# Kernel tuning notes

Measured on AMD Instinct MI355X. Metric: run time of the kernel, lower is better.

## Reference

```python
import jax, jax.numpy as jnp
import numpy as np

B, IN_DIM, OUT_DIM = 4096, 4096, 4096

def setup_inputs() -> dict:
    key = jax.random.key(0)
    kx, kw, kb = jax.random.split(key, 3)
    x = jax.random.normal(kx, (B, IN_DIM), dtype=jnp.float32)
    W = jax.random.normal(kw, (OUT_DIM, IN_DIM), dtype=jnp.float32) * (1.0 / np.sqrt(IN_DIM))
    b = jax.random.normal(kb, (OUT_DIM,), dtype=jnp.float32) * (1.0 / np.sqrt(IN_DIM))
    return {"x": x, "W": W, "b": b}

def reference(x, W, b):
    # Original computes sum over in_dim of x[:, :, None] * W.T[None, :, :],
    # which is exactly x @ W.T. NOTE: bias is added TWICE in the source
    # (duplicated `out += self.b`), so the faithful output is x @ W.T + 2*b.
    out = jnp.einsum('bi,oi->bo', x, W)  # [B, out_dim]
    out = out + 2.0 * b
    return out
```

## Files before the change

### kernel.cpp

```cpp
#include <hip/hip_runtime.h>
#include <hip/hip_bf16.h>


typedef short bf16x8 __attribute__((ext_vector_type(8)));
typedef short s16x4  __attribute__((ext_vector_type(4)));
typedef short s16x8  __attribute__((ext_vector_type(8)));
typedef float f32x4  __attribute__((ext_vector_type(4)));

constexpr int MDIM = 4096, NDIM = 4096, KDIM = 4096;

typedef const __attribute__((address_space(1))) void* gas_t;
typedef __attribute__((address_space(3))) void*       las_t;

__device__ __forceinline__ short f2bf(float f) {
    __hip_bfloat16 h = __float2bfloat16(f);
    short s; __builtin_memcpy(&s, &h, 2); return s;
}

__global__ __launch_bounds__(256)
void cvt_f32_bf16(const float* __restrict__ in, short* __restrict__ out, int n8) {
    int idx    = blockIdx.x * blockDim.x + threadIdx.x;
    int stride = gridDim.x * blockDim.x;
    const f32x4* in4 = (const f32x4*)in;
    s16x8* out8 = (s16x8*)out;
    for (int i = idx; i < n8; i += stride) {
        f32x4 a = in4[2 * i];
        f32x4 b = in4[2 * i + 1];
        s16x8 o = { f2bf(a[0]), f2bf(a[1]), f2bf(a[2]), f2bf(a[3]),
                    f2bf(b[0]), f2bf(b[1]), f2bf(b[2]), f2bf(b[3]) };
        out8[i] = o;
    }
}

constexpr int BM = 256, BN = 256, BK = 64;
constexpr int NT  = KDIM / BK;
constexpr int ASZ = BM * BK;
constexpr int BSZ = BN * BK;

template <int Q, class StageFn>
__device__ __forceinline__ void phase(const short* Ab, int rA, int c0, int c1,
                                      bf16x8 (&bf)[4][2], f32x4 (&acc)[8][4],
                                      StageFn&& stage) {
    bf16x8 af[2][2];
    #pragma unroll
    for (int m = 0; m < 2; ++m) {
        const short* p = &Ab[(rA + Q * 32 + m * 16) * BK];
        af[m][0] = *(const bf16x8*)(p + c0);
        af[m][1] = *(const bf16x8*)(p + c1);
    }
    stage();
    __builtin_amdgcn_s_barrier();
    __builtin_amdgcn_s_setprio(1);
    #pragma unroll
    for (int m = 0; m < 2; ++m)
        #pragma unroll
        for (int ni = 0; ni < 4; ++ni)
            #pragma unroll
            for (int kk = 0; kk < 2; ++kk)
                acc[Q * 2 + m][ni] = __builtin_amdgcn_mfma_f32_16x16x32_bf16(
                    af[m][kk], bf[ni][kk], acc[Q * 2 + m][ni], 0, 0, 0);
    __builtin_amdgcn_s_setprio(0);
}

__global__ __launch_bounds__(512, 2)
void gemm_bf16_256(const short* __restrict__ Xb, const short* __restrict__ Wb,
                   const float* __restrict__ Bv, float* __restrict__ Out)
{
    __shared__ short lds[2 * ASZ + 2 * BSZ];

    const int tid  = threadIdx.x;
    const int lane = tid & 63;
    const int wid  = tid >> 6;
    const int wr   = wid >> 2;
    const int wc   = wid & 3;

    const int bid = blockIdx.x;
    const int lin = (bid & 7) * 32 + (bid >> 3);
    const int tm0 = (lin >> 4) * BM;
    const int tn0 = (lin & 15) * BN;

    const int srow = lane >> 3;
    const int sgrn = (lane & 7) ^ srow;
    const short* aSrc[2][2];
    const short* bSrc[2][2];
    int dOff[2][2];
    #pragma unroll
    for (int h = 0; h < 2; ++h) {
        #pragma unroll
        for (int j = 0; j < 2; ++j) {
            const int r = h * 128 + (2 * wid + j) * 8;
            aSrc[h][j] = Xb + (size_t)(tm0 + r + srow) * KDIM + sgrn * 8;
            bSrc[h][j] = Wb + (size_t)(tn0 + r + srow) * KDIM + sgrn * 8;
            dOff[h][j] = r * BK;
        }
    }
    auto stageA = [&](int kt, int h) {
        short* dst = (short*)&lds[(kt & 1) * ASZ];
        __builtin_amdgcn_global_load_lds((gas_t)(aSrc[h][0] + (size_t)kt * BK),
                                         (las_t)(dst + dOff[h][0]), 16, 0, 0);
        __builtin_amdgcn_global_load_lds((gas_t)(aSrc[h][1] + (size_t)kt * BK),
                                         (las_t)(dst + dOff[h][1]), 16, 0, 0);
    };
    auto stageB = [&](int kt, int h) {
        short* dst = (short*)&lds[2 * ASZ + (kt & 1) * BSZ];
        __builtin_amdgcn_global_load_lds((gas_t)(bSrc[h][0] + (size_t)kt * BK),
                                         (las_t)(dst + dOff[h][0]), 16, 0, 0);
        __builtin_amdgcn_global_load_lds((gas_t)(bSrc[h][1] + (size_t)kt * BK),
                                         (las_t)(dst + dOff[h][1]), 16, 0, 0);
    };

    const int g   = lane >> 4;
    const int r16 = lane & 15;
    const int c0  = ((0 + g) ^ (r16 & 7)) * 8;
    const int c1  = ((4 + g) ^ (r16 & 7)) * 8;
    const int rA  = wr * 128 + r16;
    const int rB  = wc * 64  + r16;

    f32x4 acc[8][4] = {};

    stageB(0, 0); stageB(0, 1); stageA(0, 0); stageA(0, 1); stageB(1, 0); stageB(1, 1);
    asm volatile("s_waitcnt vmcnt(4)" ::: "memory");
    __builtin_amdgcn_s_barrier();
    __builtin_amdgcn_sched_barrier(0);

    for (int t = 0; t < NT; ++t) {
        const short* Ab = (const short*)&lds[(t & 1) * ASZ];
        const short* Bb = (const short*)&lds[2 * ASZ + (t & 1) * BSZ];

        bf16x8 bf[4][2];
        #pragma unroll
        for (int ni = 0; ni < 4; ++ni) {
            const short* p = &Bb[(rB + ni * 16) * BK];
            bf[ni][0] = *(const bf16x8*)(p + c0);
            bf[ni][1] = *(const bf16x8*)(p + c1);
        }
        phase<0>(Ab, rA, c0, c1, bf, acc, [&] { if (t + 1 < NT) stageA(t + 1, 0); });
        __builtin_amdgcn_s_barrier();
        phase<1>(Ab, rA, c0, c1, bf, acc, [&] { if (t + 1 < NT) stageA(t + 1, 1); });
        __builtin_amdgcn_s_barrier();
        phase<2>(Ab, rA, c0, c1, bf, acc, [&] { if (t + 2 < NT) stageB(t + 2, 0); });
        __builtin_amdgcn_s_barrier();
        phase<3>(Ab, rA, c0, c1, bf, acc, [&] { if (t + 2 < NT) stageB(t + 2, 1); });
        if (t < NT - 2)       { asm volatile("s_waitcnt vmcnt(4)" ::: "memory"); }
        else if (t == NT - 2) { asm volatile("s_waitcnt vmcnt(0)" ::: "memory"); }
        __builtin_amdgcn_s_barrier();
        __builtin_amdgcn_sched_barrier(0);
    }

    float bb[4];
    #pragma unroll
    for (int ni = 0; ni < 4; ++ni)
        bb[ni] = 2.0f * Bv[tn0 + wc * 64 + ni * 16 + r16];

    #pragma unroll
    for (int mi = 0; mi < 8; ++mi) {
        #pragma unroll
        for (int r = 0; r < 4; ++r) {
            const int row = tm0 + wr * 128 + mi * 16 + g * 4 + r;
            float* orow = Out + (size_t)row * NDIM + tn0 + wc * 64 + r16;
            #pragma unroll
            for (int ni = 0; ni < 4; ++ni)
                orow[ni * 16] = acc[mi][ni][r] + bb[ni];
        }
    }
}

constexpr int FBM = 128, FBN = 128, FBK = 32, LDT = FBK + 8;
__global__ __launch_bounds__(256)
void gemm_xwt_bias2(const float* __restrict__ X, const float* __restrict__ W,
                    const float* __restrict__ Bv, float* __restrict__ Out)
{
    __shared__ short As[FBM * LDT];
    __shared__ short Bs[FBN * LDT];
    const int tid  = threadIdx.x;
    const int lane = tid & 63;
    const int wid  = tid >> 6;
    const int wr   = wid >> 1;
    const int wc   = wid & 1;
    const int tm0  = blockIdx.y * FBM;
    const int tn0  = blockIdx.x * FBN;
    const int srow = tid >> 3;
    const int scol = (tid & 7) * 4;
    const int g    = lane >> 4;
    const int r16  = lane & 15;
    f32x4 acc[4][4] = {};
    const float* xg = X + (size_t)(tm0 + srow) * KDIM + scol;
    const float* wg = W + (size_t)(tn0 + srow) * KDIM + scol;
    for (int k0 = 0; k0 < KDIM; k0 += FBK) {
        #pragma unroll
        for (int i = 0; i < 4; ++i) {
            const int row = srow + 32 * i;
            f32x4 av = *(const f32x4*)(xg + (size_t)(32 * i) * KDIM + k0);
            f32x4 bv = *(const f32x4*)(wg + (size_t)(32 * i) * KDIM + k0);
            s16x4 pa = { f2bf(av[0]), f2bf(av[1]), f2bf(av[2]), f2bf(av[3]) };
            s16x4 pb = { f2bf(bv[0]), f2bf(bv[1]), f2bf(bv[2]), f2bf(bv[3]) };
            *(s16x4*)&As[row * LDT + scol] = pa;
            *(s16x4*)&Bs[row * LDT + scol] = pb;
        }
        __syncthreads();
        bf16x8 af[4], bfr[4];
        #pragma unroll
        for (int mi = 0; mi < 4; ++mi)
            af[mi] = *(const bf16x8*)&As[(wr * 64 + mi * 16 + r16) * LDT + g * 8];
        #pragma unroll
        for (int ni = 0; ni < 4; ++ni)
            bfr[ni] = *(const bf16x8*)&Bs[(wc * 64 + ni * 16 + r16) * LDT + g * 8];
        #pragma unroll
        for (int mi = 0; mi < 4; ++mi)
            #pragma unroll
            for (int ni = 0; ni < 4; ++ni)
                acc[mi][ni] = __builtin_amdgcn_mfma_f32_16x16x32_bf16(
                                  af[mi], bfr[ni], acc[mi][ni], 0, 0, 0);
        __syncthreads();
    }
    float bb[4];
    #pragma unroll
    for (int ni = 0; ni < 4; ++ni)
        bb[ni] = 2.0f * Bv[tn0 + wc * 64 + ni * 16 + r16];
    #pragma unroll
    for (int mi = 0; mi < 4; ++mi)
        #pragma unroll
        for (int r = 0; r < 4; ++r) {
            const int row = tm0 + wr * 64 + mi * 16 + g * 4 + r;
            float* orow = Out + (size_t)row * NDIM + tn0 + wc * 64 + r16;
            #pragma unroll
            for (int ni = 0; ni < 4; ++ni)
                orow[ni * 16] = acc[mi][ni][r] + bb[ni];
        }
}

extern "C" void kernel_launch(void* const* d_in, const int* in_sizes, int n_in,
                              void* d_out, int out_size, void* d_ws, size_t ws_size,
                              hipStream_t stream) {
    const float* X  = (const float*)d_in[0];
    const float* W  = (const float*)d_in[1];
    const float* Bv = (const float*)d_in[2];
    float* Out = (float*)d_out;

    const size_t nElem = (size_t)MDIM * KDIM;
    const size_t need  = 2 * nElem * sizeof(short);

    if (ws_size >= need) {
        short* Xb = (short*)d_ws;
        short* Wb = Xb + nElem;
        const int n8 = (int)(nElem / 8);
        cvt_f32_bf16<<<2048, 256, 0, stream>>>(X, Xb, n8);
        cvt_f32_bf16<<<2048, 256, 0, stream>>>(W, Wb, n8);
        gemm_bf16_256<<<dim3(256), 512, 0, stream>>>(Xb, Wb, Bv, Out);
    } else {
        dim3 grid(NDIM / FBN, MDIM / FBM);
        gemm_xwt_bias2<<<grid, 256, 0, stream>>>(X, W, Bv, Out);
    }
}
```

Before: 141.8 us.

## Switch GEMM to 32x32x16 MFMA tiles and fuse the two bf16 conversion kernels

The main GEMM now uses 32x32x16 bf16 MFMA instructions with 16-wide accumulators instead of 16x16x32, which cuts the number of LDS fragment reads per FLOP and the number of MFMA issues. The epilogue is rewritten for the 32x32 output layout. The two f32-to-bf16 conversion launches are merged into one kernel with a larger grid, saving one launch. The sched_barrier hints are dropped, which may change how the compiler interleaves LDS reads and MFMAs.

```diff
diff --git a/kernel.cpp b/kernel.cpp
--- a/kernel.cpp
+++ b/kernel.cpp
@@ -6,6 +6,7 @@
 typedef short s16x4  __attribute__((ext_vector_type(4)));
 typedef short s16x8  __attribute__((ext_vector_type(8)));
 typedef float f32x4  __attribute__((ext_vector_type(4)));
+typedef float f32x16 __attribute__((ext_vector_type(16)));
 
 constexpr int MDIM = 4096, NDIM = 4096, KDIM = 4096;
 
@@ -18,17 +19,19 @@
 }
 
 __global__ __launch_bounds__(256)
-void cvt_f32_bf16(const float* __restrict__ in, short* __restrict__ out, int n8) {
+void cvt2_f32_bf16(const float* __restrict__ inA, const float* __restrict__ inB,
+                   short* __restrict__ outA, short* __restrict__ outB, int n8each) {
     int idx    = blockIdx.x * blockDim.x + threadIdx.x;
     int stride = gridDim.x * blockDim.x;
-    const f32x4* in4 = (const f32x4*)in;
-    s16x8* out8 = (s16x8*)out;
-    for (int i = idx; i < n8; i += stride) {
-        f32x4 a = in4[2 * i];
-        f32x4 b = in4[2 * i + 1];
+    for (int i = idx; i < 2 * n8each; i += stride) {
+        const f32x4* in4 = (i < n8each) ? (const f32x4*)inA : (const f32x4*)inB;
+        s16x8*      out8 = (i < n8each) ? (s16x8*)outA      : (s16x8*)outB;
+        int j = (i < n8each) ? i : i - n8each;
+        f32x4 a = in4[2 * j];
+        f32x4 b = in4[2 * j + 1];
         s16x8 o = { f2bf(a[0]), f2bf(a[1]), f2bf(a[2]), f2bf(a[3]),
                     f2bf(b[0]), f2bf(b[1]), f2bf(b[2]), f2bf(b[3]) };
-        out8[i] = o;
+        out8[j] = o;
     }
 }
 
@@ -37,28 +40,24 @@
 constexpr int ASZ = BM * BK;
 constexpr int BSZ = BN * BK;
 
-template <int Q, class StageFn>
-__device__ __forceinline__ void phase(const short* Ab, int rA, int c0, int c1,
-                                      bf16x8 (&bf)[4][2], f32x4 (&acc)[8][4],
-                                      StageFn&& stage) {
-    bf16x8 af[2][2];
-    #pragma unroll
-    for (int m = 0; m < 2; ++m) {
-        const short* p = &Ab[(rA + Q * 32 + m * 16) * BK];
-        af[m][0] = *(const bf16x8*)(p + c0);
-        af[m][1] = *(const bf16x8*)(p + c1);
-    }
+template <int MF, class StageFn>
+__device__ __forceinline__ void phase32(const short* Ab, int rA, const int (&ck)[4],
+                                        bf16x8 (&bf)[2][4], f32x16 (&acc)[4][2],
+                                        StageFn&& stage) {
+    bf16x8 af[4];
+    const short* p = &Ab[(rA + MF * 32) * BK];
+    #pragma unroll
+    for (int s = 0; s < 4; ++s)
+        af[s] = *(const bf16x8*)(p + ck[s]);
     stage();
     __builtin_amdgcn_s_barrier();
     __builtin_amdgcn_s_setprio(1);
     #pragma unroll
-    for (int m = 0; m < 2; ++m)
-        #pragma unroll
-        for (int ni = 0; ni < 4; ++ni)
-            #pragma unroll
-            for (int kk = 0; kk < 2; ++kk)
-                acc[Q * 2 + m][ni] = __builtin_amdgcn_mfma_f32_16x16x32_bf16(
-                    af[m][kk], bf[ni][kk], acc[Q * 2 + m][ni], 0, 0, 0);
+    for (int nf = 0; nf < 2; ++nf)
+        #pragma unroll
+        for (int s = 0; s < 4; ++s)
+            acc[MF][nf] = __builtin_amdgcn_mfma_f32_32x32x16_bf16(
+                              af[s], bf[nf][s], acc[MF][nf], 0, 0, 0);
     __builtin_amdgcn_s_setprio(0);
 }
 
@@ -109,58 +108,60 @@
                                          (las_t)(dst + dOff[h][1]), 16, 0, 0);
     };
 
-    const int g   = lane >> 4;
-    const int r16 = lane & 15;
-    const int c0  = ((0 + g) ^ (r16 & 7)) * 8;
-    const int c1  = ((4 + g) ^ (r16 & 7)) * 8;
-    const int rA  = wr * 128 + r16;
-    const int rB  = wc * 64  + r16;
-
-    f32x4 acc[8][4] = {};
+    const int l31 = lane & 31;
+    const int g2  = lane >> 5;
+    int ck[4];
+    #pragma unroll
+    for (int s = 0; s < 4; ++s)
+        ck[s] = ((2 * s + g2) ^ (lane & 7)) * 8;
+    const int rA = wr * 128 + l31;
+    const int rB = wc * 64  + l31;
+
+    f32x16 acc[4][2] = {};
 
     stageB(0, 0); stageB(0, 1); stageA(0, 0); stageA(0, 1); stageB(1, 0); stageB(1, 1);
     asm volatile("s_waitcnt vmcnt(4)" ::: "memory");
     __builtin_amdgcn_s_barrier();
-    __builtin_amdgcn_sched_barrier(0);
 
     for (int t = 0; t < NT; ++t) {
         const short* Ab = (const short*)&lds[(t & 1) * ASZ];
         const short* Bb = (const short*)&lds[2 * ASZ + (t & 1) * BSZ];
 
-        bf16x8 bf[4][2];
-        #pragma unroll
-        for (int ni = 0; ni < 4; ++ni) {
-            const short* p = &Bb[(rB + ni * 16) * BK];
-            bf[ni][0] = *(const bf16x8*)(p + c0);
-            bf[ni][1] = *(const bf16x8*)(p + c1);
-        }
-        phase<0>(Ab, rA, c0, c1, bf, acc, [&] { if (t + 1 < NT) stageA(t + 1, 0); });
-        __builtin_amdgcn_s_barrier();
-        phase<1>(Ab, rA, c0, c1, bf, acc, [&] { if (t + 1 < NT) stageA(t + 1, 1); });
-        __builtin_amdgcn_s_barrier();
-        phase<2>(Ab, rA, c0, c1, bf, acc, [&] { if (t + 2 < NT) stageB(t + 2, 0); });
-        __builtin_amdgcn_s_barrier();
-        phase<3>(Ab, rA, c0, c1, bf, acc, [&] { if (t + 2 < NT) stageB(t + 2, 1); });
+        bf16x8 bf[2][4];
+        #pragma unroll
+        for (int nf = 0; nf < 2; ++nf) {
+            const short* p = &Bb[(rB + nf * 32) * BK];
+            #pragma unroll
+            for (int s = 0; s < 4; ++s)
+                bf[nf][s] = *(const bf16x8*)(p + ck[s]);
+        }
+        phase32<0>(Ab, rA, ck, bf, acc, [&] { if (t + 1 < NT) stageA(t + 1, 0); });
+        __builtin_amdgcn_s_barrier();
+        phase32<1>(Ab, rA, ck, bf, acc, [&] { if (t + 1 < NT) stageA(t + 1, 1); });
+        __builtin_amdgcn_s_barrier();
+        phase32<2>(Ab, rA, ck, bf, acc, [&] { if (t + 2 < NT) stageB(t + 2, 0); });
+        __builtin_amdgcn_s_barrier();
+        phase32<3>(Ab, rA, ck, bf, acc, [&] { if (t + 2 < NT) stageB(t + 2, 1); });
         if (t < NT - 2)       { asm volatile("s_waitcnt vmcnt(4)" ::: "memory"); }
         else if (t == NT - 2) { asm volatile("s_waitcnt vmcnt(0)" ::: "memory"); }
         __builtin_amdgcn_s_barrier();
-        __builtin_amdgcn_sched_barrier(0);
-    }
-
-    float bb[4];
-    #pragma unroll
-    for (int ni = 0; ni < 4; ++ni)
-        bb[ni] = 2.0f * Bv[tn0 + wc * 64 + ni * 16 + r16];
-
-    #pragma unroll
-    for (int mi = 0; mi < 8; ++mi) {
-        #pragma unroll
-        for (int r = 0; r < 4; ++r) {
-            const int row = tm0 + wr * 128 + mi * 16 + g * 4 + r;
-            float* orow = Out + (size_t)row * NDIM + tn0 + wc * 64 + r16;
-            #pragma unroll
-            for (int ni = 0; ni < 4; ++ni)
-                orow[ni * 16] = acc[mi][ni][r] + bb[ni];
+    }
+
+    float bb[2];
+    #pragma unroll
+    for (int nf = 0; nf < 2; ++nf)
+        bb[nf] = 2.0f * Bv[tn0 + wc * 64 + nf * 32 + l31];
+
+    #pragma unroll
+    for (int mf = 0; mf < 4; ++mf) {
+        #pragma unroll
+        for (int reg = 0; reg < 16; ++reg) {
+            const int row = tm0 + wr * 128 + mf * 32
+                          + (reg & 3) + 8 * (reg >> 2) + 4 * g2;
+            float* orow = Out + (size_t)row * NDIM + tn0 + wc * 64 + l31;
+            #pragma unroll
+            for (int nf = 0; nf < 2; ++nf)
+                orow[nf * 32] = acc[mf][nf][reg] + bb[nf];
         }
     }
 }
@@ -244,8 +245,7 @@
         short* Xb = (short*)d_ws;
         short* Wb = Xb + nElem;
         const int n8 = (int)(nElem / 8);
-        cvt_f32_bf16<<<2048, 256, 0, stream>>>(X, Xb, n8);
-        cvt_f32_bf16<<<2048, 256, 0, stream>>>(W, Wb, n8);
+        cvt2_f32_bf16<<<4096, 256, 0, stream>>>(X, W, Xb, Wb, n8);
         gemm_bf16_256<<<dim3(256), 512, 0, stream>>>(Xb, Wb, Bv, Out);
     } else {
         dim3 grid(NDIM / FBN, MDIM / FBM);
```

Result: slower. 155.3 us (+9.5%).
